# Kernel tuning notes

Hardware: AMD Instinct MI355X
Metric: run time of the kernel (lower is better)

The kernel has to match this reference:

```python
import jax, jax.numpy as jnp
import numpy as np

N, K, M, S = 131072, 64, 64, 128


def setup_inputs() -> dict:
    key = jax.random.key(0)
    kA, kB, kS = jax.random.split(key, 3)
    mat_A = jax.random.normal(kA, (N, K), dtype=jnp.float32)
    mat_B = jax.random.normal(kB, (S, K, M), dtype=jnp.float32)
    segment_id_A = jnp.sort(jax.random.randint(kS, (N,), 0, S, dtype=jnp.int64))
    segment_id_B = jnp.arange(S, dtype=jnp.int64)
    return {"mat_A": mat_A, "mat_B": mat_B,
            "segment_id_A": segment_id_A, "segment_id_B": segment_id_B}


def reference(mat_A, mat_B, segment_id_A, segment_id_B):
    # segment_id_B labels the S segment matrices in mat_B; remap so that
    # position j of B_eff corresponds to segment label j (identity when
    # segment_id_B == arange(S)).
    B_eff = jnp.zeros_like(mat_B).at[segment_id_B].set(mat_B)  # [S, K, M]
    # Grouped GEMM: out[i] = mat_A[i] @ B_eff[segment_id_A[i]]
    # expressed as a batched matvec over N rows (gather + contraction on K).
    out = jnp.einsum('nk,nkm->nm', mat_A, B_eff[segment_id_A])  # [N, M]
    return out
```

## Files before the change

kernel.cpp:

```cpp
#include <hip/hip_runtime.h>


typedef float f32x4 __attribute__((ext_vector_type(4)));
typedef short s16x8 __attribute__((ext_vector_type(8)));

#define WPB 4
#define RPW 32

__global__ void build_inv_kernel(const int* __restrict__ segB, int* __restrict__ inv, int S) {
    int j = threadIdx.x + blockIdx.x * blockDim.x;
    if (j < S) inv[segB[j]] = j;
}

__device__ __forceinline__ short f2bf(float f) {
    unsigned u = __builtin_bit_cast(unsigned, f);
    u += 0x7fffu + ((u >> 16) & 1u);
    return (short)(u >> 16);
}

__global__ __launch_bounds__(256, 4) void segmm_mfma(
        const float* __restrict__ A,
        const float* __restrict__ B,
        const int*   __restrict__ segA,
        const int*   __restrict__ inv,
        float*       __restrict__ out,
        int nrows) {
    const int lane  = threadIdx.x & 63;
    const int row16 = lane & 15;
    const int kgrp  = lane >> 4;

    int w  = blockIdx.x * WPB + (threadIdx.x >> 6);
    int r0 = __builtin_amdgcn_readfirstlane(w * RPW);
    if (r0 >= nrows) return;

    s16x8 bf00, bf01, bf10, bf11, bf20, bf21, bf30, bf31;
    int j_cur = -1;

    #pragma unroll
    for (int t = 0; t < RPW / 16; ++t) {
        const int rt = r0 + 16 * t;
        const int s0 = __builtin_amdgcn_readfirstlane(segA[rt]);
        const int s1 = __builtin_amdgcn_readfirstlane(segA[rt + 15]);

        if (s0 == s1) {
            const int j = __builtin_amdgcn_readfirstlane(inv[s0]);
            if (j != j_cur) {
                j_cur = j;
                const float* __restrict__ bp = B + (size_t)j * 4096;
                const int col = row16;
                #define LOADB(frag, ct, ks) do {                                  \
                    s16x8 f;                                                      \
                    const float* q = bp + (size_t)(kgrp * 8 + (ks) * 32) * 64     \
                                        + (ct) * 16 + col;                        \
                    _Pragma("unroll")                                             \
                    for (int i = 0; i < 8; ++i) f[i] = f2bf(q[(size_t)i * 64]);   \
                    frag = f; } while (0)
                LOADB(bf00, 0, 0); LOADB(bf01, 0, 1);
                LOADB(bf10, 1, 0); LOADB(bf11, 1, 1);
                LOADB(bf20, 2, 0); LOADB(bf21, 2, 1);
                LOADB(bf30, 3, 0); LOADB(bf31, 3, 1);
                #undef LOADB
                asm volatile("" : "+v"(bf00), "+v"(bf01), "+v"(bf10), "+v"(bf11),
                                  "+v"(bf20), "+v"(bf21), "+v"(bf30), "+v"(bf31));
            }

            s16x8 af0, af1;
            {
                const float* __restrict__ ap =
                    A + (size_t)(rt + row16) * 64 + kgrp * 8;
                f32x4 lo = *(const f32x4*)(ap);
                f32x4 hi = *(const f32x4*)(ap + 4);
                af0[0]=f2bf(lo[0]); af0[1]=f2bf(lo[1]); af0[2]=f2bf(lo[2]); af0[3]=f2bf(lo[3]);
                af0[4]=f2bf(hi[0]); af0[5]=f2bf(hi[1]); af0[6]=f2bf(hi[2]); af0[7]=f2bf(hi[3]);
                f32x4 lo2 = *(const f32x4*)(ap + 32);
                f32x4 hi2 = *(const f32x4*)(ap + 36);
                af1[0]=f2bf(lo2[0]); af1[1]=f2bf(lo2[1]); af1[2]=f2bf(lo2[2]); af1[3]=f2bf(lo2[3]);
                af1[4]=f2bf(hi2[0]); af1[5]=f2bf(hi2[1]); af1[6]=f2bf(hi2[2]); af1[7]=f2bf(hi2[3]);
            }

            #define DOTILE(b0, b1, ct) do {                                       \
                f32x4 acc = {0.f, 0.f, 0.f, 0.f};                                 \
                acc = __builtin_amdgcn_mfma_f32_16x16x32_bf16(af0, b0, acc, 0,0,0);\
                acc = __builtin_amdgcn_mfma_f32_16x16x32_bf16(af1, b1, acc, 0,0,0);\
                _Pragma("unroll")                                                 \
                for (int reg = 0; reg < 4; ++reg)                                 \
                    out[(size_t)(rt + kgrp * 4 + reg) * 64 + (ct) * 16 + row16]   \
                        = acc[reg];                                               \
            } while (0)
            DOTILE(bf00, bf01, 0);
            DOTILE(bf10, bf11, 1);
            DOTILE(bf20, bf21, 2);
            DOTILE(bf30, bf31, 3);
            #undef DOTILE
        } else {
            for (int r = rt; r < rt + 16; ++r) {
                const int s = __builtin_amdgcn_readfirstlane(segA[r]);
                const int j = __builtin_amdgcn_readfirstlane(inv[s]);
                const float* __restrict__ ap = A + (size_t)r * 64;
                const float* __restrict__ bp = B + (size_t)j * 4096 + lane;
                float a0 = 0.f, a1 = 0.f, a2 = 0.f, a3 = 0.f;
                #pragma unroll
                for (int k = 0; k < 64; k += 4) {
                    a0 = fmaf(ap[k + 0], bp[(size_t)(k + 0) * 64], a0);
                    a1 = fmaf(ap[k + 1], bp[(size_t)(k + 1) * 64], a1);
                    a2 = fmaf(ap[k + 2], bp[(size_t)(k + 2) * 64], a2);
                    a3 = fmaf(ap[k + 3], bp[(size_t)(k + 3) * 64], a3);
                }
                out[(size_t)r * 64 + lane] = (a0 + a1) + (a2 + a3);
            }
        }
    }
}

extern "C" void kernel_launch(void* const* d_in, const int* in_sizes, int n_in,
                              void* d_out, int out_size, void* d_ws, size_t ws_size,
                              hipStream_t stream) {
    const float* A    = (const float*)d_in[0];
    const float* B    = (const float*)d_in[1];
    const int*   segA = (const int*)d_in[2];
    const int*   segB = (const int*)d_in[3];
    float*       out  = (float*)d_out;
    int*         inv  = (int*)d_ws;

    const int K = 64;
    const int N = in_sizes[0] / K;
    const int S = in_sizes[3];

    build_inv_kernel<<<(S + 127) / 128, 128, 0, stream>>>(segB, inv, S);

    int waves  = (N + RPW - 1) / RPW;
    int blocks = (waves + WPB - 1) / WPB;
    segmm_mfma<<<blocks, 256, 0, stream>>>(A, B, segA, inv, out, N);
}
```

Before: 107.6 us.

## Process 64 rows per wave with batched loads and transposed MFMA output

Each wave now handles 64 rows. When all of them share one segment, the wave issues every B and A load up front, then converts them and runs 16 MFMA tiles. Swapping the MFMA operands transposes the output fragment, so each lane writes a contiguous f32x4 instead of scalar strided stores. The aim is more memory-level parallelism and vectorized stores. In exchange, register pressure rises (launch bounds drop to 2 blocks per SIMD), and waves that straddle a segment boundary fall back to the per-16-row path.

```diff
diff --git a/kernel.cpp b/kernel.cpp
--- a/kernel.cpp
+++ b/kernel.cpp
@@ -5,7 +5,7 @@
 typedef short s16x8 __attribute__((ext_vector_type(8)));
 
 #define WPB 4
-#define RPW 32
+#define RPW 64
 
 __global__ void build_inv_kernel(const int* __restrict__ segB, int* __restrict__ inv, int S) {
     int j = threadIdx.x + blockIdx.x * blockDim.x;
@@ -18,95 +18,147 @@
     return (short)(u >> 16);
 }
 
-__global__ __launch_bounds__(256, 4) void segmm_mfma(
+__global__ __launch_bounds__(256, 2) void segmm_mfma(
         const float* __restrict__ A,
         const float* __restrict__ B,
         const int*   __restrict__ segA,
         const int*   __restrict__ inv,
         float*       __restrict__ out,
         int nrows) {
-    const int lane  = threadIdx.x & 63;
-    const int row16 = lane & 15;
-    const int kgrp  = lane >> 4;
+    const int lane = threadIdx.x & 63;
+    const int n16  = lane & 15;
+    const int kg   = lane >> 4;
 
     int w  = blockIdx.x * WPB + (threadIdx.x >> 6);
     int r0 = __builtin_amdgcn_readfirstlane(w * RPW);
     if (r0 >= nrows) return;
 
-    s16x8 bf00, bf01, bf10, bf11, bf20, bf21, bf30, bf31;
-    int j_cur = -1;
+    const bool whole = (r0 + RPW <= nrows);
+    const int  sFirst = __builtin_amdgcn_readfirstlane(segA[r0]);
+    const int  sLast  = whole ? __builtin_amdgcn_readfirstlane(segA[r0 + RPW - 1]) : -1;
 
-    #pragma unroll
-    for (int t = 0; t < RPW / 16; ++t) {
-        const int rt = r0 + 16 * t;
-        const int s0 = __builtin_amdgcn_readfirstlane(segA[rt]);
-        const int s1 = __builtin_amdgcn_readfirstlane(segA[rt + 15]);
+    if (whole && sFirst == sLast) {
+        const int j = __builtin_amdgcn_readfirstlane(inv[sFirst]);
 
-        if (s0 == s1) {
-            const int j = __builtin_amdgcn_readfirstlane(inv[s0]);
-            if (j != j_cur) {
-                j_cur = j;
-                const float* __restrict__ bp = B + (size_t)j * 4096;
-                const int col = row16;
-                #define LOADB(frag, ct, ks) do {                                  \
-                    s16x8 f;                                                      \
-                    const float* q = bp + (size_t)(kgrp * 8 + (ks) * 32) * 64     \
-                                        + (ct) * 16 + col;                        \
-                    _Pragma("unroll")                                             \
-                    for (int i = 0; i < 8; ++i) f[i] = f2bf(q[(size_t)i * 64]);   \
-                    frag = f; } while (0)
-                LOADB(bf00, 0, 0); LOADB(bf01, 0, 1);
-                LOADB(bf10, 1, 0); LOADB(bf11, 1, 1);
-                LOADB(bf20, 2, 0); LOADB(bf21, 2, 1);
-                LOADB(bf30, 3, 0); LOADB(bf31, 3, 1);
-                #undef LOADB
-                asm volatile("" : "+v"(bf00), "+v"(bf01), "+v"(bf10), "+v"(bf11),
-                                  "+v"(bf20), "+v"(bf21), "+v"(bf30), "+v"(bf31));
+        const float* __restrict__ bbase = B + (size_t)j * 4096 + n16;
+        float br[4][2][8];
+        #pragma unroll
+        for (int ct = 0; ct < 4; ++ct)
+            #pragma unroll
+            for (int ks = 0; ks < 2; ++ks)
+                #pragma unroll
+                for (int i = 0; i < 8; ++i)
+                    br[ct][ks][i] = bbase[(size_t)(kg * 8 + i + ks * 32) * 64 + ct * 16];
+
+        const float* __restrict__ abase = A + (size_t)(r0 + n16) * 64 + kg * 8;
+        f32x4 ar[4][2][2];
+        #pragma unroll
+        for (int t = 0; t < 4; ++t)
+            #pragma unroll
+            for (int ks = 0; ks < 2; ++ks)
+                #pragma unroll
+                for (int h = 0; h < 2; ++h)
+                    ar[t][ks][h] = *(const f32x4*)(abase + t * 1024 + ks * 32 + h * 4);
+
+        s16x8 bfr[4][2];
+        #pragma unroll
+        for (int ct = 0; ct < 4; ++ct)
+            #pragma unroll
+            for (int ks = 0; ks < 2; ++ks)
+                #pragma unroll
+                for (int i = 0; i < 8; ++i)
+                    bfr[ct][ks][i] = f2bf(br[ct][ks][i]);
+
+        s16x8 af[4][2];
+        #pragma unroll
+        for (int t = 0; t < 4; ++t)
+            #pragma unroll
+            for (int ks = 0; ks < 2; ++ks) {
+                #pragma unroll
+                for (int i = 0; i < 4; ++i) {
+                    af[t][ks][i]     = f2bf(ar[t][ks][0][i]);
+                    af[t][ks][i + 4] = f2bf(ar[t][ks][1][i]);
+                }
             }
 
-            s16x8 af0, af1;
-            {
-                const float* __restrict__ ap =
-                    A + (size_t)(rt + row16) * 64 + kgrp * 8;
-                f32x4 lo = *(const f32x4*)(ap);
-                f32x4 hi = *(const f32x4*)(ap + 4);
-                af0[0]=f2bf(lo[0]); af0[1]=f2bf(lo[1]); af0[2]=f2bf(lo[2]); af0[3]=f2bf(lo[3]);
-                af0[4]=f2bf(hi[0]); af0[5]=f2bf(hi[1]); af0[6]=f2bf(hi[2]); af0[7]=f2bf(hi[3]);
-                f32x4 lo2 = *(const f32x4*)(ap + 32);
-                f32x4 hi2 = *(const f32x4*)(ap + 36);
-                af1[0]=f2bf(lo2[0]); af1[1]=f2bf(lo2[1]); af1[2]=f2bf(lo2[2]); af1[3]=f2bf(lo2[3]);
-                af1[4]=f2bf(hi2[0]); af1[5]=f2bf(hi2[1]); af1[6]=f2bf(hi2[2]); af1[7]=f2bf(hi2[3]);
+        #pragma unroll
+        for (int t = 0; t < 4; ++t) {
+            #pragma unroll
+            for (int ct = 0; ct < 4; ++ct) {
+                f32x4 acc = {0.f, 0.f, 0.f, 0.f};
+                acc = __builtin_amdgcn_mfma_f32_16x16x32_bf16(bfr[ct][0], af[t][0], acc, 0, 0, 0);
+                acc = __builtin_amdgcn_mfma_f32_16x16x32_bf16(bfr[ct][1], af[t][1], acc, 0, 0, 0);
+                *(f32x4*)(out + (size_t)(r0 + t * 16 + n16) * 64 + ct * 16 + kg * 4) = acc;
             }
+        }
+    } else {
+        int j_cur = -1;
+        s16x8 bfr[4][2];
+        for (int t = 0; t < RPW / 16; ++t) {
+            const int rt = r0 + 16 * t;
+            if (rt >= nrows) break;
+            const bool full = (rt + 16 <= nrows);
+            const int sa = __builtin_amdgcn_readfirstlane(segA[rt]);
+            const int sb = full ? __builtin_amdgcn_readfirstlane(segA[rt + 15]) : -1;
 
-            #define DOTILE(b0, b1, ct) do {                                       \
-                f32x4 acc = {0.f, 0.f, 0.f, 0.f};                                 \
-                acc = __builtin_amdgcn_mfma_f32_16x16x32_bf16(af0, b0, acc, 0,0,0);\
-                acc = __builtin_amdgcn_mfma_f32_16x16x32_bf16(af1, b1, acc, 0,0,0);\
-                _Pragma("unroll")                                                 \
-                for (int reg = 0; reg < 4; ++reg)                                 \
-                    out[(size_t)(rt + kgrp * 4 + reg) * 64 + (ct) * 16 + row16]   \
-                        = acc[reg];                                               \
-            } while (0)
-            DOTILE(bf00, bf01, 0);
-            DOTILE(bf10, bf11, 1);
-            DOTILE(bf20, bf21, 2);
-            DOTILE(bf30, bf31, 3);
-            #undef DOTILE
-        } else {
-            for (int r = rt; r < rt + 16; ++r) {
-                const int s = __builtin_amdgcn_readfirstlane(segA[r]);
-                const int j = __builtin_amdgcn_readfirstlane(inv[s]);
-                const float* __restrict__ ap = A + (size_t)r * 64;
-                const float* __restrict__ bp = B + (size_t)j * 4096 + lane;
-                float a0 = 0.f, a1 = 0.f, a2 = 0.f, a3 = 0.f;
+            if (full && sa == sb) {
+                const int j = __builtin_amdgcn_readfirstlane(inv[sa]);
+                if (j != j_cur) {
+                    j_cur = j;
+                    const float* __restrict__ bbase = B + (size_t)j * 4096 + n16;
+                    #pragma unroll
+                    for (int ct = 0; ct < 4; ++ct)
+                        #pragma unroll
+                        for (int ks = 0; ks < 2; ++ks) {
+                            float tmp[8];
+                            #pragma unroll
+                            for (int i = 0; i < 8; ++i)
+                                tmp[i] = bbase[(size_t)(kg * 8 + i + ks * 32) * 64 + ct * 16];
+                            #pragma unroll
+                            for (int i = 0; i < 8; ++i)
+                                bfr[ct][ks][i] = f2bf(tmp[i]);
+                        }
+                }
+                const float* __restrict__ ap = A + (size_t)(rt + n16) * 64 + kg * 8;
+                s16x8 af0, af1;
+                {
+                    f32x4 lo  = *(const f32x4*)(ap);
+                    f32x4 hi  = *(const f32x4*)(ap + 4);
+                    f32x4 lo2 = *(const f32x4*)(ap + 32);
+                    f32x4 hi2 = *(const f32x4*)(ap + 36);
+                    #pragma unroll
+                    for (int i = 0; i < 4; ++i) {
+                        af0[i]     = f2bf(lo[i]);
+                        af0[i + 4] = f2bf(hi[i]);
+                        af1[i]     = f2bf(lo2[i]);
+                        af1[i + 4] = f2bf(hi2[i]);
+                    }
+                }
                 #pragma unroll
-                for (int k = 0; k < 64; k += 4) {
-                    a0 = fmaf(ap[k + 0], bp[(size_t)(k + 0) * 64], a0);
-                    a1 = fmaf(ap[k + 1], bp[(size_t)(k + 1) * 64], a1);
-                    a2 = fmaf(ap[k + 2], bp[(size_t)(k + 2) * 64], a2);
-                    a3 = fmaf(ap[k + 3], bp[(size_t)(k + 3) * 64], a3);
+                for (int ct = 0; ct < 4; ++ct) {
+                    f32x4 acc = {0.f, 0.f, 0.f, 0.f};
+                    acc = __builtin_amdgcn_mfma_f32_16x16x32_bf16(bfr[ct][0], af0, acc, 0, 0, 0);
+                    acc = __builtin_amdgcn_mfma_f32_16x16x32_bf16(bfr[ct][1], af1, acc, 0, 0, 0);
+                    *(f32x4*)(out + (size_t)(rt + n16) * 64 + ct * 16 + kg * 4) = acc;
                 }
-                out[(size_t)r * 64 + lane] = (a0 + a1) + (a2 + a3);
+            } else {
+                const int rEnd = full ? rt + 16 : nrows;
+                for (int r = rt; r < rEnd; ++r) {
+                    const int s = __builtin_amdgcn_readfirstlane(segA[r]);
+                    const int j = __builtin_amdgcn_readfirstlane(inv[s]);
+                    const float* __restrict__ ap = A + (size_t)r * 64;
+                    const float* __restrict__ bp = B + (size_t)j * 4096 + lane;
+                    float a0 = 0.f, a1 = 0.f, a2 = 0.f, a3 = 0.f;
+                    #pragma unroll
+                    for (int k = 0; k < 64; k += 4) {
+                        a0 = fmaf(ap[k + 0], bp[(size_t)(k + 0) * 64], a0);
+                        a1 = fmaf(ap[k + 1], bp[(size_t)(k + 1) * 64], a1);
+                        a2 = fmaf(ap[k + 2], bp[(size_t)(k + 2) * 64], a2);
+                        a3 = fmaf(ap[k + 3], bp[(size_t)(k + 3) * 64], a3);
+                    }
+                    out[(size_t)r * 64 + lane] = (a0 + a1) + (a2 + a3);
+                }
+                j_cur = -1;
             }
         }
     }
```

Measured after the change: 114.1 us. +6.0%, slower.
